# Performance work log

Hardware: AMD Instinct MI355X
Metric: run time of the kernel (lower is better)

The kernel has to match this reference:

```python
import jax, jax.numpy as jnp
import numpy as np

B, Q, K, CQ, CK, CV, H, C, CO = 2, 2048, 2048, 256, 256, 256, 8, 32, 256

def setup_inputs() -> dict:
    key = jax.random.key(0)
    ks = jax.random.split(key, 12)
    s_in = 1.0 / np.sqrt(CQ)
    return {
        "q_x": jax.random.normal(ks[0], (B, Q, CQ), jnp.float32),
        "kv_x": jax.random.normal(ks[1], (B, K, CK), jnp.float32),
        "bias1": jax.random.normal(ks[2], (B, H, Q, K), jnp.float32),
        "bias2": jax.random.normal(ks[3], (B, H, Q, K), jnp.float32),
        "Wq": jax.random.normal(ks[4], (CQ, H * C), jnp.float32) * s_in,
        "Wk": jax.random.normal(ks[5], (CK, H * C), jnp.float32) * s_in,
        "Wv": jax.random.normal(ks[6], (CV, H * C), jnp.float32) * s_in,
        "Wg": jax.random.normal(ks[7], (CQ, H * C), jnp.float32) * 0.02,
        "bg": jnp.ones((H * C,), jnp.float32),
        "Wo": jax.random.normal(ks[8], (H * C, CO), jnp.float32) * 0.02,
        "bo": jnp.zeros((CO,), jnp.float32),
    }

def reference(q_x, kv_x, bias1, bias2, Wq, Wk, Wv, Wg, bg, Wo, bo):
    # project and split heads: [B, L, H*C] -> [B, H, L, C]
    def heads(x):
        return x.reshape(x.shape[0], x.shape[1], H, C).transpose(0, 2, 1, 3)
    q = heads(q_x @ Wq) * (C ** -0.5)
    k = heads(kv_x @ Wk)
    v = heads(kv_x @ Wv)
    # QK^T + additive pair biases, softmax, PV
    a = jnp.einsum("bhqc,bhkc->bhqk", q, k) + bias1 + bias2
    a = jax.nn.softmax(a, axis=-1)
    o = jnp.einsum("bhqk,bhkc->bhqc", a, v)
    o = o.transpose(0, 2, 1, 3)  # [B, Q, H, C]
    # sigmoid gating from query data
    g = jax.nn.sigmoid(q_x @ Wg + bg).reshape(B, Q, H, C)
    o = (o * g).reshape(B, Q, H * C)
    return o @ Wo + bo
```

## Files before the change

kernel.cpp:

```cpp
#include <hip/hip_runtime.h>
#include <math.h>

#define NB 2
#define NQ 2048
#define NK 2048
#define NH 8
#define NC 32
#define NHC 256
#define NCIN 256

__device__ __forceinline__ float redmax16(float v) {
    v = fmaxf(v, __shfl_xor(v, 1, 16));
    v = fmaxf(v, __shfl_xor(v, 2, 16));
    v = fmaxf(v, __shfl_xor(v, 4, 16));
    v = fmaxf(v, __shfl_xor(v, 8, 16));
    return v;
}
__device__ __forceinline__ float redsum16(float v) {
    v += __shfl_xor(v, 1, 16);
    v += __shfl_xor(v, 2, 16);
    v += __shfl_xor(v, 4, 16);
    v += __shfl_xor(v, 8, 16);
    return v;
}

__device__ __forceinline__ void gemm_tile(const float* __restrict__ A,
                                          const float* __restrict__ W,
                                          float (*__restrict__ As)[68],
                                          float (*__restrict__ Bs)[68],
                                          float acc[4][4], int m0, int n0)
{
    const int t = threadIdx.x;
    const int ty = t >> 4, tx = t & 15;
    const int arow = t >> 2, acol = (t & 3) * 8;
    const int brow = t >> 3, bcol = (t & 7) * 8;

    for (int k0 = 0; k0 < NCIN; k0 += 32) {
        float4 a0 = *(const float4*)&A[(size_t)(m0 + arow) * NCIN + k0 + acol];
        float4 a1 = *(const float4*)&A[(size_t)(m0 + arow) * NCIN + k0 + acol + 4];
        float4 b0 = *(const float4*)&W[(size_t)(k0 + brow) * NHC + n0 + bcol];
        float4 b1 = *(const float4*)&W[(size_t)(k0 + brow) * NHC + n0 + bcol + 4];
        __syncthreads();
        As[acol + 0][arow] = a0.x; As[acol + 1][arow] = a0.y;
        As[acol + 2][arow] = a0.z; As[acol + 3][arow] = a0.w;
        As[acol + 4][arow] = a1.x; As[acol + 5][arow] = a1.y;
        As[acol + 6][arow] = a1.z; As[acol + 7][arow] = a1.w;
        *(float4*)&Bs[brow][bcol]     = b0;
        *(float4*)&Bs[brow][bcol + 4] = b1;
        __syncthreads();
        #pragma unroll
        for (int kk = 0; kk < 32; ++kk) {
            float4 av = *(const float4*)&As[kk][ty * 4];
            float4 bv = *(const float4*)&Bs[kk][tx * 4];
            float a_[4] = {av.x, av.y, av.z, av.w};
            float b_[4] = {bv.x, bv.y, bv.z, bv.w};
            #pragma unroll
            for (int i = 0; i < 4; ++i)
                #pragma unroll
                for (int j = 0; j < 4; ++j)
                    acc[i][j] = fmaf(a_[i], b_[j], acc[i][j]);
        }
    }
}

__global__ __launch_bounds__(256) void proj_kernel(
    const float* __restrict__ q_x, const float* __restrict__ kv_x,
    const float* __restrict__ Wq, const float* __restrict__ Wk,
    const float* __restrict__ Wv, const float* __restrict__ Wg,
    const float* __restrict__ bg,
    float* __restrict__ qh, float* __restrict__ kh,
    float* __restrict__ vh, float* __restrict__ gh)
{
    __shared__ float As[32][68];
    __shared__ float Bs[32][68];
    const int mode = blockIdx.z;
    const float* A = (mode == 0 || mode == 3) ? q_x : kv_x;
    const float* W = (mode == 0) ? Wq : (mode == 1) ? Wk : (mode == 2) ? Wv : Wg;
    float* out = (mode == 0) ? qh : (mode == 1) ? kh : (mode == 2) ? vh : gh;
    const int m0 = blockIdx.x * 64, n0 = blockIdx.y * 64;

    float acc[4][4] = {};
    gemm_tile(A, W, As, Bs, acc, m0, n0);

    const int t = threadIdx.x, ty = t >> 4, tx = t & 15;
    #pragma unroll
    for (int i = 0; i < 4; ++i) {
        const int m = m0 + ty * 4 + i;
        const int b = m >> 11, l = m & 2047;
        const int n = n0 + tx * 4;
        const int h = n >> 5, c = n & 31;
        float v[4];
        #pragma unroll
        for (int j = 0; j < 4; ++j) v[j] = acc[i][j];
        if (mode == 0) {
            #pragma unroll
            for (int j = 0; j < 4; ++j) v[j] *= 0.17677669529663687f;
        } else if (mode == 3) {
            #pragma unroll
            for (int j = 0; j < 4; ++j)
                v[j] = 1.0f / (1.0f + __expf(-(v[j] + bg[n + j])));
        }
        float4 vv; vv.x = v[0]; vv.y = v[1]; vv.z = v[2]; vv.w = v[3];
        *(float4*)&out[((size_t)(b * NH + h) * NQ + l) * NC + c] = vv;
    }
}

__global__ __launch_bounds__(256) void out_proj_kernel(
    const float* __restrict__ og, const float* __restrict__ Wo,
    const float* __restrict__ bo, float* __restrict__ out)
{
    __shared__ float As[32][68];
    __shared__ float Bs[32][68];
    const int m0 = blockIdx.x * 64, n0 = blockIdx.y * 64;
    float acc[4][4] = {};
    gemm_tile(og, Wo, As, Bs, acc, m0, n0);
    const int t = threadIdx.x, ty = t >> 4, tx = t & 15;
    #pragma unroll
    for (int i = 0; i < 4; ++i) {
        const int m = m0 + ty * 4 + i;
        const int n = n0 + tx * 4;
        float4 bv = *(const float4*)&bo[n];
        float4 vv;
        vv.x = acc[i][0] + bv.x; vv.y = acc[i][1] + bv.y;
        vv.z = acc[i][2] + bv.z; vv.w = acc[i][3] + bv.w;
        *(float4*)&out[(size_t)m * NHC + n] = vv;
    }
}

__global__ __launch_bounds__(256) void attn_kernel(
    const float* __restrict__ qh, const float* __restrict__ kh,
    const float* __restrict__ vh, const float* __restrict__ gh,
    const float* __restrict__ b1, const float* __restrict__ b2,
    float* __restrict__ og)
{
    __shared__ float qT[32][68];
    __shared__ float kT[32][68];
    __shared__ float vs[64][36];
    __shared__ float pT[64][68];

    const int wg  = blockIdx.x;
    const int xcd = wg & 7;
    const int idx = wg >> 3;
    const int bh  = xcd * 2 + (idx >> 5);
    const int qt  = idx & 31;
    const int q0  = qt * 64;

    const int t  = threadIdx.x;
    const int ty = t >> 4, tx = t & 15;
    const int sr = t >> 2, sc = (t & 3) * 8;

    {
        const float* qb = qh + ((size_t)bh * NQ + q0) * NC;
        float4 x0 = *(const float4*)&qb[sr * NC + sc];
        float4 x1 = *(const float4*)&qb[sr * NC + sc + 4];
        qT[sc + 0][sr] = x0.x; qT[sc + 1][sr] = x0.y;
        qT[sc + 2][sr] = x0.z; qT[sc + 3][sr] = x0.w;
        qT[sc + 4][sr] = x1.x; qT[sc + 5][sr] = x1.y;
        qT[sc + 6][sr] = x1.z; qT[sc + 7][sr] = x1.w;
    }

    float m_run[4], l_run[4], o_acc[4][2];
    #pragma unroll
    for (int i = 0; i < 4; ++i) {
        m_run[i] = -3.0e38f; l_run[i] = 0.0f;
        o_acc[i][0] = 0.0f; o_acc[i][1] = 0.0f;
    }

    const float* kb = kh + (size_t)bh * NK * NC;
    const float* vb = vh + (size_t)bh * NK * NC;
    const size_t brow0 = (size_t)bh * NQ + q0;

    float4 kx0 = *(const float4*)&kb[(size_t)sr * NC + sc];
    float4 kx1 = *(const float4*)&kb[(size_t)sr * NC + sc + 4];
    float4 vx0 = *(const float4*)&vb[(size_t)sr * NC + sc];
    float4 vx1 = *(const float4*)&vb[(size_t)sr * NC + sc + 4];
    float4 nb1[4], nb2[4];
    #pragma unroll
    for (int i = 0; i < 4; ++i) {
        const size_t off = (brow0 + ty * 4 + i) * (size_t)NK + tx * 4;
        nb1[i] = *(const float4*)&b1[off];
        nb2[i] = *(const float4*)&b2[off];
    }

    for (int kt = 0; kt < NK / 64; ++kt) {
        const int kk0 = kt * 64;
        __syncthreads();
        kT[sc + 0][sr] = kx0.x; kT[sc + 1][sr] = kx0.y;
        kT[sc + 2][sr] = kx0.z; kT[sc + 3][sr] = kx0.w;
        kT[sc + 4][sr] = kx1.x; kT[sc + 5][sr] = kx1.y;
        kT[sc + 6][sr] = kx1.z; kT[sc + 7][sr] = kx1.w;
        *(float4*)&vs[sr][sc]     = vx0;
        *(float4*)&vs[sr][sc + 4] = vx1;
        __syncthreads();

        float4 cb1[4], cb2[4];
        #pragma unroll
        for (int i = 0; i < 4; ++i) { cb1[i] = nb1[i]; cb2[i] = nb2[i]; }

        if (kt + 1 < NK / 64) {
            const size_t noff = (size_t)(kk0 + 64 + sr) * NC + sc;
            kx0 = *(const float4*)&kb[noff];
            kx1 = *(const float4*)&kb[noff + 4];
            vx0 = *(const float4*)&vb[noff];
            vx1 = *(const float4*)&vb[noff + 4];
            #pragma unroll
            for (int i = 0; i < 4; ++i) {
                const size_t off =
                    (brow0 + ty * 4 + i) * (size_t)NK + kk0 + 64 + tx * 4;
                nb1[i] = *(const float4*)&b1[off];
                nb2[i] = *(const float4*)&b2[off];
            }
        }

        float s[4][4] = {};
        #pragma unroll
        for (int c = 0; c < 32; ++c) {
            float4 av = *(const float4*)&qT[c][ty * 4];
            float4 kv = *(const float4*)&kT[c][tx * 4];
            float a_[4] = {av.x, av.y, av.z, av.w};
            float k_[4] = {kv.x, kv.y, kv.z, kv.w};
            #pragma unroll
            for (int i = 0; i < 4; ++i)
                #pragma unroll
                for (int j = 0; j < 4; ++j)
                    s[i][j] = fmaf(a_[i], k_[j], s[i][j]);
        }

        float p[4][4];
        #pragma unroll
        for (int i = 0; i < 4; ++i) {
            s[i][0] += cb1[i].x + cb2[i].x;
            s[i][1] += cb1[i].y + cb2[i].y;
            s[i][2] += cb1[i].z + cb2[i].z;
            s[i][3] += cb1[i].w + cb2[i].w;
            float tm = fmaxf(fmaxf(s[i][0], s[i][1]), fmaxf(s[i][2], s[i][3]));
            tm = redmax16(tm);
            const float mn   = fmaxf(m_run[i], tm);
            const float resc = __expf(m_run[i] - mn);
            p[i][0] = __expf(s[i][0] - mn);
            p[i][1] = __expf(s[i][1] - mn);
            p[i][2] = __expf(s[i][2] - mn);
            p[i][3] = __expf(s[i][3] - mn);
            const float tsum = redsum16(p[i][0] + p[i][1] + p[i][2] + p[i][3]);
            l_run[i] = l_run[i] * resc + tsum;
            o_acc[i][0] *= resc; o_acc[i][1] *= resc;
            m_run[i] = mn;
        }
        #pragma unroll
        for (int j = 0; j < 4; ++j) {
            float4 w;
            w.x = p[0][j]; w.y = p[1][j]; w.z = p[2][j]; w.w = p[3][j];
            *(float4*)&pT[tx * 4 + j][ty * 4] = w;
        }
        __syncthreads();

        #pragma unroll
        for (int k = 0; k < 64; ++k) {
            float4 p4 = *(const float4*)&pT[k][ty * 4];
            float2 v2 = *(const float2*)&vs[k][tx * 2];
            o_acc[0][0] = fmaf(p4.x, v2.x, o_acc[0][0]);
            o_acc[0][1] = fmaf(p4.x, v2.y, o_acc[0][1]);
            o_acc[1][0] = fmaf(p4.y, v2.x, o_acc[1][0]);
            o_acc[1][1] = fmaf(p4.y, v2.y, o_acc[1][1]);
            o_acc[2][0] = fmaf(p4.z, v2.x, o_acc[2][0]);
            o_acc[2][1] = fmaf(p4.z, v2.y, o_acc[2][1]);
            o_acc[3][0] = fmaf(p4.w, v2.x, o_acc[3][0]);
            o_acc[3][1] = fmaf(p4.w, v2.y, o_acc[3][1]);
        }
    }

    const int b = bh >> 3, h = bh & 7;
    #pragma unroll
    for (int i = 0; i < 4; ++i) {
        const int r = q0 + ty * 4 + i;
        const float inv = 1.0f / l_run[i];
        float2 g2 = *(const float2*)&gh[((size_t)bh * NQ + r) * NC + tx * 2];
        float2 o2;
        o2.x = o_acc[i][0] * inv * g2.x;
        o2.y = o_acc[i][1] * inv * g2.y;
        *(float2*)&og[((size_t)(b * NQ + r)) * NHC + h * NC + tx * 2] = o2;
    }
}

extern "C" void kernel_launch(void* const* d_in, const int* in_sizes, int n_in,
                              void* d_out, int out_size, void* d_ws, size_t ws_size,
                              hipStream_t stream) {
    const float* q_x   = (const float*)d_in[0];
    const float* kv_x  = (const float*)d_in[1];
    const float* bias1 = (const float*)d_in[2];
    const float* bias2 = (const float*)d_in[3];
    const float* Wq    = (const float*)d_in[4];
    const float* Wk    = (const float*)d_in[5];
    const float* Wv    = (const float*)d_in[6];
    const float* Wg    = (const float*)d_in[7];
    const float* bg    = (const float*)d_in[8];
    const float* Wo    = (const float*)d_in[9];
    const float* bo    = (const float*)d_in[10];
    float* out = (float*)d_out;

    float* ws = (float*)d_ws;
    const size_t SEG = (size_t)NB * NH * NQ * NC;
    float* qh = ws;
    float* kh = ws + SEG;
    float* vh = ws + 2 * SEG;
    float* gh = ws + 3 * SEG;
    float* og = ws + 4 * SEG;

    proj_kernel<<<dim3(64, 4, 4), 256, 0, stream>>>(q_x, kv_x, Wq, Wk, Wv, Wg, bg,
                                                    qh, kh, vh, gh);
    attn_kernel<<<dim3(512), 256, 0, stream>>>(qh, kh, vh, gh, bias1, bias2, og);
    out_proj_kernel<<<dim3(64, 4), 256, 0, stream>>>(og, Wo, bo, out);
}
```

Baseline: 640.1 us.

## Use bf16 MFMA for attention QK and PV with transposed V layout

Projections now write Q and K in bf16 and V transposed in bf16. The attention kernel replaces its scalar FP32 shared-memory dot products with 16x16x32 bf16 MFMA instructions: each wave computes 16 query rows, and P is staged through a small per-wave LDS buffer. K and V fragments are loaded straight from global memory without block-wide syncs. This aims to cut FP32 ALU time in attention, but it lowers precision to bf16 and reads the bias tensors with scalar, less-coalesced loads.

```diff
diff --git a/kernel.cpp b/kernel.cpp
--- a/kernel.cpp
+++ b/kernel.cpp
@@ -1,4 +1,5 @@
 #include <hip/hip_runtime.h>
+#include <hip/hip_bf16.h>
 #include <math.h>
 
 #define NB 2
@@ -8,6 +9,9 @@
 #define NC 32
 #define NHC 256
 #define NCIN 256
+
+typedef short bf16x8 __attribute__((ext_vector_type(8)));
+typedef float f32x4 __attribute__((ext_vector_type(4)));
 
 __device__ __forceinline__ float redmax16(float v) {
     v = fmaxf(v, __shfl_xor(v, 1, 16));
@@ -68,40 +72,54 @@
     const float* __restrict__ Wq, const float* __restrict__ Wk,
     const float* __restrict__ Wv, const float* __restrict__ Wg,
     const float* __restrict__ bg,
-    float* __restrict__ qh, float* __restrict__ kh,
-    float* __restrict__ vh, float* __restrict__ gh)
+    __hip_bfloat16* __restrict__ qh, __hip_bfloat16* __restrict__ kh,
+    __hip_bfloat16* __restrict__ vt, float* __restrict__ gh)
 {
     __shared__ float As[32][68];
     __shared__ float Bs[32][68];
     const int mode = blockIdx.z;
     const float* A = (mode == 0 || mode == 3) ? q_x : kv_x;
     const float* W = (mode == 0) ? Wq : (mode == 1) ? Wk : (mode == 2) ? Wv : Wg;
-    float* out = (mode == 0) ? qh : (mode == 1) ? kh : (mode == 2) ? vh : gh;
     const int m0 = blockIdx.x * 64, n0 = blockIdx.y * 64;
 
     float acc[4][4] = {};
     gemm_tile(A, W, As, Bs, acc, m0, n0);
 
     const int t = threadIdx.x, ty = t >> 4, tx = t & 15;
-    #pragma unroll
-    for (int i = 0; i < 4; ++i) {
-        const int m = m0 + ty * 4 + i;
-        const int b = m >> 11, l = m & 2047;
-        const int n = n0 + tx * 4;
-        const int h = n >> 5, c = n & 31;
-        float v[4];
-        #pragma unroll
-        for (int j = 0; j < 4; ++j) v[j] = acc[i][j];
-        if (mode == 0) {
-            #pragma unroll
-            for (int j = 0; j < 4; ++j) v[j] *= 0.17677669529663687f;
-        } else if (mode == 3) {
-            #pragma unroll
-            for (int j = 0; j < 4; ++j)
-                v[j] = 1.0f / (1.0f + __expf(-(v[j] + bg[n + j])));
-        }
-        float4 vv; vv.x = v[0]; vv.y = v[1]; vv.z = v[2]; vv.w = v[3];
-        *(float4*)&out[((size_t)(b * NH + h) * NQ + l) * NC + c] = vv;
+    const int m  = m0 + ty * 4;
+    const int b  = m >> 11, ll = m & 2047;
+    const int n  = n0 + tx * 4;
+    const int hh = n >> 5,  cc = n & 31;
+    const int bhn = b * NH + hh;
+
+    if (mode == 0 || mode == 1) {
+        __hip_bfloat16* dst = (mode == 0) ? qh : kh;
+        const float sc = (mode == 0) ? 0.17677669529663687f : 1.0f;
+        #pragma unroll
+        for (int i = 0; i < 4; ++i) {
+            __hip_bfloat16 h4[4];
+            #pragma unroll
+            for (int j = 0; j < 4; ++j) h4[j] = __float2bfloat16(acc[i][j] * sc);
+            *(uint2*)&dst[((size_t)bhn * NQ + ll + i) * NC + cc] = *(uint2*)h4;
+        }
+    } else if (mode == 2) {
+        #pragma unroll
+        for (int j = 0; j < 4; ++j) {
+            __hip_bfloat16 h4[4];
+            #pragma unroll
+            for (int i = 0; i < 4; ++i) h4[i] = __float2bfloat16(acc[i][j]);
+            *(uint2*)&vt[((size_t)bhn * NC + cc + j) * NQ + ll] = *(uint2*)h4;
+        }
+    } else {
+        #pragma unroll
+        for (int i = 0; i < 4; ++i) {
+            float4 vv;
+            vv.x = 1.0f / (1.0f + __expf(-(acc[i][0] + bg[n + 0])));
+            vv.y = 1.0f / (1.0f + __expf(-(acc[i][1] + bg[n + 1])));
+            vv.z = 1.0f / (1.0f + __expf(-(acc[i][2] + bg[n + 2])));
+            vv.w = 1.0f / (1.0f + __expf(-(acc[i][3] + bg[n + 3])));
+            *(float4*)&gh[((size_t)bhn * NQ + ll + i) * NC + cc] = vv;
+        }
     }
 }
 
@@ -128,157 +146,134 @@
 }
 
 __global__ __launch_bounds__(256) void attn_kernel(
-    const float* __restrict__ qh, const float* __restrict__ kh,
-    const float* __restrict__ vh, const float* __restrict__ gh,
+    const __hip_bfloat16* __restrict__ qh, const __hip_bfloat16* __restrict__ kh,
+    const __hip_bfloat16* __restrict__ vt, const float* __restrict__ gh,
     const float* __restrict__ b1, const float* __restrict__ b2,
     float* __restrict__ og)
 {
-    __shared__ float qT[32][68];
-    __shared__ float kT[32][68];
-    __shared__ float vs[64][36];
-    __shared__ float pT[64][68];
+    __shared__ __align__(16) __hip_bfloat16 p_lds[2][4][16][88];
 
     const int wg  = blockIdx.x;
     const int xcd = wg & 7;
     const int idx = wg >> 3;
     const int bh  = xcd * 2 + (idx >> 5);
-    const int qt  = idx & 31;
-    const int q0  = qt * 64;
-
-    const int t  = threadIdx.x;
-    const int ty = t >> 4, tx = t & 15;
-    const int sr = t >> 2, sc = (t & 3) * 8;
-
-    {
-        const float* qb = qh + ((size_t)bh * NQ + q0) * NC;
-        float4 x0 = *(const float4*)&qb[sr * NC + sc];
-        float4 x1 = *(const float4*)&qb[sr * NC + sc + 4];
-        qT[sc + 0][sr] = x0.x; qT[sc + 1][sr] = x0.y;
-        qT[sc + 2][sr] = x0.z; qT[sc + 3][sr] = x0.w;
-        qT[sc + 4][sr] = x1.x; qT[sc + 5][sr] = x1.y;
-        qT[sc + 6][sr] = x1.z; qT[sc + 7][sr] = x1.w;
-    }
-
-    float m_run[4], l_run[4], o_acc[4][2];
+    const int q0  = (idx & 31) * 64;
+
+    const int tid = threadIdx.x;
+    const int w   = tid >> 6;
+    const int l   = tid & 63;
+    const int l15 = l & 15;
+    const int g   = l >> 4;
+
+    const bf16x8 qa = *reinterpret_cast<const bf16x8*>(
+        &qh[((size_t)bh * NQ + q0 + 16 * w + l15) * NC + 8 * g]);
+
+    float m_run[4], l_run[4];
+    f32x4 o_acc[2];
     #pragma unroll
-    for (int i = 0; i < 4; ++i) {
-        m_run[i] = -3.0e38f; l_run[i] = 0.0f;
-        o_acc[i][0] = 0.0f; o_acc[i][1] = 0.0f;
-    }
-
-    const float* kb = kh + (size_t)bh * NK * NC;
-    const float* vb = vh + (size_t)bh * NK * NC;
-    const size_t brow0 = (size_t)bh * NQ + q0;
-
-    float4 kx0 = *(const float4*)&kb[(size_t)sr * NC + sc];
-    float4 kx1 = *(const float4*)&kb[(size_t)sr * NC + sc + 4];
-    float4 vx0 = *(const float4*)&vb[(size_t)sr * NC + sc];
-    float4 vx1 = *(const float4*)&vb[(size_t)sr * NC + sc + 4];
-    float4 nb1[4], nb2[4];
+    for (int r = 0; r < 4; ++r) { m_run[r] = -3.0e38f; l_run[r] = 0.0f; }
+    o_acc[0] = (f32x4){0.f, 0.f, 0.f, 0.f};
+    o_acc[1] = (f32x4){0.f, 0.f, 0.f, 0.f};
+
+    const __hip_bfloat16* kbase = kh + (size_t)bh * NK * NC;
+    const __hip_bfloat16* vbase = vt + (size_t)bh * NC * NK;
+    const size_t brow = (size_t)bh * NQ + q0 + 16 * w;
+
+    float nb1[4][4], nb2[4][4];
     #pragma unroll
-    for (int i = 0; i < 4; ++i) {
-        const size_t off = (brow0 + ty * 4 + i) * (size_t)NK + tx * 4;
-        nb1[i] = *(const float4*)&b1[off];
-        nb2[i] = *(const float4*)&b2[off];
-    }
+    for (int r = 0; r < 4; ++r)
+        #pragma unroll
+        for (int t = 0; t < 4; ++t) {
+            const size_t off = (brow + 4 * g + r) * (size_t)NK + 16 * t + l15;
+            nb1[r][t] = b1[off];
+            nb2[r][t] = b2[off];
+        }
 
     for (int kt = 0; kt < NK / 64; ++kt) {
         const int kk0 = kt * 64;
-        __syncthreads();
-        kT[sc + 0][sr] = kx0.x; kT[sc + 1][sr] = kx0.y;
-        kT[sc + 2][sr] = kx0.z; kT[sc + 3][sr] = kx0.w;
-        kT[sc + 4][sr] = kx1.x; kT[sc + 5][sr] = kx1.y;
-        kT[sc + 6][sr] = kx1.z; kT[sc + 7][sr] = kx1.w;
-        *(float4*)&vs[sr][sc]     = vx0;
-        *(float4*)&vs[sr][sc + 4] = vx1;
-        __syncthreads();
-
-        float4 cb1[4], cb2[4];
-        #pragma unroll
-        for (int i = 0; i < 4; ++i) { cb1[i] = nb1[i]; cb2[i] = nb2[i]; }
-
-        if (kt + 1 < NK / 64) {
-            const size_t noff = (size_t)(kk0 + 64 + sr) * NC + sc;
-            kx0 = *(const float4*)&kb[noff];
-            kx1 = *(const float4*)&kb[noff + 4];
-            vx0 = *(const float4*)&vb[noff];
-            vx1 = *(const float4*)&vb[noff + 4];
-            #pragma unroll
-            for (int i = 0; i < 4; ++i) {
-                const size_t off =
-                    (brow0 + ty * 4 + i) * (size_t)NK + kk0 + 64 + tx * 4;
-                nb1[i] = *(const float4*)&b1[off];
-                nb2[i] = *(const float4*)&b2[off];
+        bf16x8 kf[4];
+        #pragma unroll
+        for (int t = 0; t < 4; ++t)
+            kf[t] = *reinterpret_cast<const bf16x8*>(
+                &kbase[(size_t)(kk0 + 16 * t + l15) * NC + 8 * g]);
+        bf16x8 vf[2][2];
+        #pragma unroll
+        for (int n = 0; n < 2; ++n)
+            #pragma unroll
+            for (int ks = 0; ks < 2; ++ks)
+                vf[n][ks] = *reinterpret_cast<const bf16x8*>(
+                    &vbase[(size_t)(16 * n + l15) * NK + kk0 + 32 * ks + 8 * g]);
+
+        f32x4 dqk[4];
+        #pragma unroll
+        for (int t = 0; t < 4; ++t)
+            dqk[t] = __builtin_amdgcn_mfma_f32_16x16x32_bf16(
+                qa, kf[t], (f32x4){0.f, 0.f, 0.f, 0.f}, 0, 0, 0);
+
+        float p[4][4], resc[4];
+        #pragma unroll
+        for (int r = 0; r < 4; ++r) {
+            float s0 = dqk[0][r] + nb1[r][0] + nb2[r][0];
+            float s1 = dqk[1][r] + nb1[r][1] + nb2[r][1];
+            float s2 = dqk[2][r] + nb1[r][2] + nb2[r][2];
+            float s3 = dqk[3][r] + nb1[r][3] + nb2[r][3];
+            float tm = redmax16(fmaxf(fmaxf(s0, s1), fmaxf(s2, s3)));
+            const float mn = fmaxf(m_run[r], tm);
+            resc[r] = __expf(m_run[r] - mn);
+            p[r][0] = __expf(s0 - mn);
+            p[r][1] = __expf(s1 - mn);
+            p[r][2] = __expf(s2 - mn);
+            p[r][3] = __expf(s3 - mn);
+            const float ts = redsum16(p[r][0] + p[r][1] + p[r][2] + p[r][3]);
+            l_run[r] = l_run[r] * resc[r] + ts;
+            m_run[r] = mn;
+        }
+        #pragma unroll
+        for (int n = 0; n < 2; ++n)
+            #pragma unroll
+            for (int r = 0; r < 4; ++r)
+                o_acc[n][r] *= resc[r];
+
+        const int pb = kt & 1;
+        #pragma unroll
+        for (int r = 0; r < 4; ++r)
+            #pragma unroll
+            for (int t = 0; t < 4; ++t)
+                p_lds[pb][w][4 * g + r][16 * t + l15] = __float2bfloat16(p[r][t]);
+
+        const int nk0 = (kt + 1 < NK / 64) ? kk0 + 64 : 0;
+        #pragma unroll
+        for (int r = 0; r < 4; ++r)
+            #pragma unroll
+            for (int t = 0; t < 4; ++t) {
+                const size_t off = (brow + 4 * g + r) * (size_t)NK + nk0 + 16 * t + l15;
+                nb1[r][t] = b1[off];
+                nb2[r][t] = b2[off];
             }
-        }
-
-        float s[4][4] = {};
-        #pragma unroll
-        for (int c = 0; c < 32; ++c) {
-            float4 av = *(const float4*)&qT[c][ty * 4];
-            float4 kv = *(const float4*)&kT[c][tx * 4];
-            float a_[4] = {av.x, av.y, av.z, av.w};
-            float k_[4] = {kv.x, kv.y, kv.z, kv.w};
-            #pragma unroll
-            for (int i = 0; i < 4; ++i)
-                #pragma unroll
-                for (int j = 0; j < 4; ++j)
-                    s[i][j] = fmaf(a_[i], k_[j], s[i][j]);
-        }
-
-        float p[4][4];
-        #pragma unroll
-        for (int i = 0; i < 4; ++i) {
-            s[i][0] += cb1[i].x + cb2[i].x;
-            s[i][1] += cb1[i].y + cb2[i].y;
-            s[i][2] += cb1[i].z + cb2[i].z;
-            s[i][3] += cb1[i].w + cb2[i].w;
-            float tm = fmaxf(fmaxf(s[i][0], s[i][1]), fmaxf(s[i][2], s[i][3]));
-            tm = redmax16(tm);
-            const float mn   = fmaxf(m_run[i], tm);
-            const float resc = __expf(m_run[i] - mn);
-            p[i][0] = __expf(s[i][0] - mn);
-            p[i][1] = __expf(s[i][1] - mn);
-            p[i][2] = __expf(s[i][2] - mn);
-            p[i][3] = __expf(s[i][3] - mn);
-            const float tsum = redsum16(p[i][0] + p[i][1] + p[i][2] + p[i][3]);
-            l_run[i] = l_run[i] * resc + tsum;
-            o_acc[i][0] *= resc; o_acc[i][1] *= resc;
-            m_run[i] = mn;
-        }
-        #pragma unroll
-        for (int j = 0; j < 4; ++j) {
-            float4 w;
-            w.x = p[0][j]; w.y = p[1][j]; w.z = p[2][j]; w.w = p[3][j];
-            *(float4*)&pT[tx * 4 + j][ty * 4] = w;
-        }
-        __syncthreads();
-
-        #pragma unroll
-        for (int k = 0; k < 64; ++k) {
-            float4 p4 = *(const float4*)&pT[k][ty * 4];
-            float2 v2 = *(const float2*)&vs[k][tx * 2];
-            o_acc[0][0] = fmaf(p4.x, v2.x, o_acc[0][0]);
-            o_acc[0][1] = fmaf(p4.x, v2.y, o_acc[0][1]);
-            o_acc[1][0] = fmaf(p4.y, v2.x, o_acc[1][0]);
-            o_acc[1][1] = fmaf(p4.y, v2.y, o_acc[1][1]);
-            o_acc[2][0] = fmaf(p4.z, v2.x, o_acc[2][0]);
-            o_acc[2][1] = fmaf(p4.z, v2.y, o_acc[2][1]);
-            o_acc[3][0] = fmaf(p4.w, v2.x, o_acc[3][0]);
-            o_acc[3][1] = fmaf(p4.w, v2.y, o_acc[3][1]);
-        }
+
+        asm volatile("s_waitcnt lgkmcnt(0)" ::: "memory");
+        __builtin_amdgcn_sched_barrier(0);
+
+        const bf16x8 pa0 = *reinterpret_cast<const bf16x8*>(&p_lds[pb][w][l15][8 * g]);
+        const bf16x8 pa1 = *reinterpret_cast<const bf16x8*>(&p_lds[pb][w][l15][32 + 8 * g]);
+
+        o_acc[0] = __builtin_amdgcn_mfma_f32_16x16x32_bf16(pa0, vf[0][0], o_acc[0], 0, 0, 0);
+        o_acc[0] = __builtin_amdgcn_mfma_f32_16x16x32_bf16(pa1, vf[0][1], o_acc[0], 0, 0, 0);
+        o_acc[1] = __builtin_amdgcn_mfma_f32_16x16x32_bf16(pa0, vf[1][0], o_acc[1], 0, 0, 0);
+        o_acc[1] = __builtin_amdgcn_mfma_f32_16x16x32_bf16(pa1, vf[1][1], o_acc[1], 0, 0, 0);
     }
 
     const int b = bh >> 3, h = bh & 7;
     #pragma unroll
-    for (int i = 0; i < 4; ++i) {
-        const int r = q0 + ty * 4 + i;
-        const float inv = 1.0f / l_run[i];
-        float2 g2 = *(const float2*)&gh[((size_t)bh * NQ + r) * NC + tx * 2];
-        float2 o2;
-        o2.x = o_acc[i][0] * inv * g2.x;
-        o2.y = o_acc[i][1] * inv * g2.y;
-        *(float2*)&og[((size_t)(b * NQ + r)) * NHC + h * NC + tx * 2] = o2;
+    for (int r = 0; r < 4; ++r) {
+        const int grow = q0 + 16 * w + 4 * g + r;
+        const float inv = 1.0f / l_run[r];
+        #pragma unroll
+        for (int n = 0; n < 2; ++n) {
+            const int c = 16 * n + l15;
+            const float gate = gh[((size_t)bh * NQ + grow) * NC + c];
+            og[((size_t)(b * NQ + grow)) * NHC + h * NC + c] = o_acc[n][r] * inv * gate;
+        }
     }
 }
 
@@ -298,16 +293,16 @@
     const float* bo    = (const float*)d_in[10];
     float* out = (float*)d_out;
 
-    float* ws = (float*)d_ws;
-    const size_t SEG = (size_t)NB * NH * NQ * NC;
-    float* qh = ws;
-    float* kh = ws + SEG;
-    float* vh = ws + 2 * SEG;
-    float* gh = ws + 3 * SEG;
-    float* og = ws + 4 * SEG;
+    char* ws = (char*)d_ws;
+    const size_t NTOK = (size_t)NB * NH * NQ * NC;
+    __hip_bfloat16* qh = (__hip_bfloat16*)(ws);
+    __hip_bfloat16* kh = (__hip_bfloat16*)(ws + 2 * NTOK);
+    __hip_bfloat16* vt = (__hip_bfloat16*)(ws + 4 * NTOK);
+    float*          gh = (float*)         (ws + 6 * NTOK);
+    float*          og = (float*)         (ws + 10 * NTOK);
 
     proj_kernel<<<dim3(64, 4, 4), 256, 0, stream>>>(q_x, kv_x, Wq, Wk, Wv, Wg, bg,
-                                                    qh, kh, vh, gh);
-    attn_kernel<<<dim3(512), 256, 0, stream>>>(qh, kh, vh, gh, bias1, bias2, og);
+                                                    qh, kh, vt, gh);
+    attn_kernel<<<dim3(512), 256, 0, stream>>>(qh, kh, vt, gh, bias1, bias2, og);
     out_proj_kernel<<<dim3(64, 4), 256, 0, stream>>>(og, Wo, bo, out);
 }
```

Result: faster. 589.3 us (-7.9%).
